# Optimization experiments

Measured on AMD Instinct MI355X. Metric: run time of the kernel, lower is better.

## Reference

```python
import jax, jax.numpy as jnp
import numpy as np

N_NODES = 50000
N_EDGES = 1600000
NODE_DIM = 64
HID = 16


def setup_inputs() -> dict:
    key = jax.random.key(0)
    ks = jax.random.split(key, 12)
    f = lambda k, shape: (jax.random.normal(k, shape, dtype=jnp.float32) * 0.1)
    edge_index = jax.random.randint(ks[0], (2, N_EDGES), 0, N_NODES)
    return {
        "edge_index": edge_index,
        "node_emb": f(ks[1], (N_NODES, NODE_DIM)),
        "edge_emb": f(ks[2], (N_EDGES, HID)),
        "W1": f(ks[3], (NODE_DIM, HID)),
        "att_src1": f(ks[4], (HID,)),
        "att_dst1": f(ks[5], (HID,)),
        "b1": jnp.zeros((HID,), jnp.float32),
        "W2": f(ks[6], (HID, HID)),
        "att_src2": f(ks[7], (HID,)),
        "att_dst2": f(ks[8], (HID,)),
        "b2": jnp.zeros((HID,), jnp.float32),
        "Wm1": f(ks[9], (3 * HID, HID)),
        "bm1": jnp.zeros((HID,), jnp.float32),
        "Wm2": f(ks[10], (HID, 1)),
        "bm2": jnp.zeros((1,), jnp.float32),
    }


def gat_layer(x, src, dst, W, a_src, a_dst, b, num_nodes):
    # Single-head GATConv (PyG defaults): self-loops, leaky_relu(0.2), softmax over dst.
    h = x @ W  # [N, out]
    logits = jax.nn.leaky_relu((h @ a_src)[src] + (h @ a_dst)[dst], negative_slope=0.2)
    m = jax.ops.segment_max(logits, dst, num_segments=num_nodes)  # stable softmax
    e = jnp.exp(logits - jax.lax.stop_gradient(m)[dst])
    denom = jax.ops.segment_sum(e, dst, num_segments=num_nodes)
    coef = e / denom[dst]  # [E+N]
    out = jax.ops.segment_sum(coef[:, None] * h[src], dst, num_segments=num_nodes)
    return out + b


def reference(edge_index, node_emb, edge_emb, W1, att_src1, att_dst1, b1,
              W2, att_src2, att_dst2, b2, Wm1, bm1, Wm2, bm2):
    src, dst = edge_index[0], edge_index[1]
    num_nodes = node_emb.shape[0]
    loops = jnp.arange(num_nodes)
    src_f = jnp.concatenate([src, loops])  # GATConv add_self_loops=True
    dst_f = jnp.concatenate([dst, loops])

    x = node_emb
    for (W, a_s, a_d, b) in [(W1, att_src1, att_dst1, b1), (W2, att_src2, att_dst2, b2)]:
        x = gat_layer(x, src_f, dst_f, W, a_s, a_d, b, num_nodes)
        x = jax.nn.gelu(x, approximate=False)  # torch F.gelu default = exact erf
        # dropout omitted (eval mode)

    # Vectorized replacement of the per-edge Python loop:
    edge_repr = jnp.concatenate([x[src], x[dst], edge_emb], axis=1)  # [E, 3*HID]
    hmid = jax.nn.relu(edge_repr @ Wm1 + bm1)
    probs = jax.nn.sigmoid(hmid @ Wm2 + bm2)[:, 0]  # [E]
    return probs
```

## Files before the change

kernel.cpp:

```cpp
#include <hip/hip_runtime.h>
#include <math.h>

#define N_NODES 50000
#define N_EDGES 1600000
#define NODE_DIM 64
#define HID 16
#define BSZ 64
#define NBUCK ((N_NODES + BSZ - 1) / BSZ)
#define CAPB 2560
#define EPB 2048
#define APB 256
#define APPEND_BLOCKS ((N_EDGES + EPB - 1) / EPB)

typedef _Float16 h8 __attribute__((ext_vector_type(8)));

__global__ void append_kernel(const int* __restrict__ ei,
                              int* __restrict__ gcount,
                              unsigned int* __restrict__ blist) {
    __shared__ int lcount[NBUCK];
    __shared__ int gbase[NBUCK];
    __shared__ int loff[NBUCK];
    int t = threadIdx.x;
    for (int b = t; b < NBUCK; b += APB) { lcount[b] = 0; loff[b] = 0; }
    __syncthreads();
    long base = (long)blockIdx.x * EPB;
#pragma unroll
    for (int k = 0; k < EPB / APB; k++) {
        long i = base + k * APB + t;
        if (i < N_EDGES) atomicAdd(&lcount[ei[N_EDGES + i] >> 6], 1);
    }
    __syncthreads();
    for (int b = t; b < NBUCK; b += APB) {
        int c = lcount[b];
        gbase[b] = c ? atomicAdd(&gcount[b], c) : 0;
    }
    __syncthreads();
#pragma unroll
    for (int k = 0; k < EPB / APB; k++) {
        long i = base + k * APB + t;
        if (i < N_EDGES) {
            int s = ei[i], d = ei[N_EDGES + i];
            int b = d >> 6;
            int pos = gbase[b] + atomicAdd(&loff[b], 1);
            if (pos < CAPB)
                blist[(size_t)b * CAPB + pos] = ((unsigned)(d & 63) << 16) | (unsigned)s;
        }
    }
}

__global__ void sort_kernel(const int* __restrict__ gcount, const unsigned int* __restrict__ blist,
                            unsigned short* __restrict__ csr, int* __restrict__ dstbeg) {
    __shared__ int cnts[BSZ];
    __shared__ int sc[BSZ];
    __shared__ int off[BSZ];
    int b = blockIdx.x, t = threadIdx.x;
    if (t < BSZ) cnts[t] = 0;
    __syncthreads();
    int cnt = gcount[b]; if (cnt > CAPB) cnt = CAPB;
    const unsigned int* lp = blist + (size_t)b * CAPB;
    for (int k = t; k < cnt; k += APB) atomicAdd(&cnts[lp[k] >> 16], 1);
    __syncthreads();
    if (t < BSZ) sc[t] = cnts[t];
    __syncthreads();
    for (int o = 1; o < BSZ; o <<= 1) {
        int v = 0;
        if (t < BSZ && t >= o) v = sc[t - o];
        __syncthreads();
        if (t < BSZ) sc[t] += v;
        __syncthreads();
    }
    if (t < BSZ) {
        int beg = sc[t] - cnts[t];
        off[t] = beg;
        dstbeg[(b << 6) + t] = beg;
    }
    __syncthreads();
    for (int k = t; k < cnt; k += APB) {
        unsigned int r = lp[k];
        int pos = atomicAdd(&off[r >> 16], 1);
        csr[(size_t)b * CAPB + pos] = (unsigned short)(r & 0xFFFF);
    }
}

__global__ void node_h64(const float* __restrict__ x,
                         const float* __restrict__ W,
                         const float* __restrict__ a_src,
                         const float* __restrict__ a_dst,
                         float* __restrict__ h,
                         float* __restrict__ as_, float* __restrict__ ad_) {
    int t = threadIdx.x;
    int n = blockIdx.x * blockDim.x + t;
    if (n >= N_NODES) return;
    float acc[HID];
#pragma unroll
    for (int j = 0; j < HID; j++) acc[j] = 0.f;
    const float4* xr = (const float4*)(x + (size_t)n * NODE_DIM);
#pragma unroll
    for (int k4 = 0; k4 < NODE_DIM / 4; k4++) {
        float4 xv = xr[k4];
        const float* w0 = W + (k4 * 4) * HID;
#pragma unroll
        for (int j = 0; j < HID; j++)
            acc[j] += xv.x * w0[j] + xv.y * w0[HID + j] + xv.z * w0[2 * HID + j] + xv.w * w0[3 * HID + j];
    }
    float s = 0.f, d = 0.f;
#pragma unroll
    for (int j = 0; j < HID; j++) {
        h[(size_t)n * HID + j] = acc[j];
        s += acc[j] * a_src[j];
        d += acc[j] * a_dst[j];
    }
    as_[n] = s; ad_[n] = d;
}

__global__ void gather1_fused(const int* __restrict__ gcount, const int* __restrict__ dstbeg,
                              const unsigned short* __restrict__ csr,
                              const float* __restrict__ h,
                              const float* __restrict__ as_, const float* __restrict__ ad_,
                              const float* __restrict__ b,
                              const float* __restrict__ W2,
                              const float* __restrict__ a_src2,
                              const float* __restrict__ a_dst2,
                              float* __restrict__ h2out,
                              float* __restrict__ as2, float* __restrict__ ad2) {
    int t = threadIdx.x;
    int j = t & 15;
    int half = (t >> 4) & 1;
    float Wcol[HID];
#pragma unroll
    for (int k = 0; k < HID; k++) Wcol[k] = W2[k * HID + j];
    float a2j = a_src2[j], d2j = a_dst2[j], bj = b[j];
    int g = blockIdx.x * (blockDim.x >> 5) + (t >> 5);
    if (g >= N_NODES) return;
    int bk = g >> 6, dl = g & 63;
    int cnt_b = gcount[bk]; if (cnt_b > CAPB) cnt_b = CAPB;
    int beg = dstbeg[g];
    int end = (dl < 63) ? dstbeg[g + 1] : cnt_b;
    if (end > cnt_b) end = cnt_b;
    if (beg > end) beg = end;
    const unsigned short* row = csr + (size_t)bk * CAPB + beg;
    int cnt = end - beg;
    int ch = (cnt + 1) >> 1;
    int lo = half ? ch : 0;
    int hi = half ? cnt : ch;
    float adn = ad_[g];
    float acc = 0.f, den = 0.f;
    int k = lo;
    for (; k + 4 <= hi; k += 4) {
        int s0 = row[k], s1 = row[k + 1], s2 = row[k + 2], s3 = row[k + 3];
        float l0 = as_[s0] + adn, l1 = as_[s1] + adn;
        float l2 = as_[s2] + adn, l3 = as_[s3] + adn;
        l0 = l0 > 0.f ? l0 : 0.2f * l0;
        l1 = l1 > 0.f ? l1 : 0.2f * l1;
        l2 = l2 > 0.f ? l2 : 0.2f * l2;
        l3 = l3 > 0.f ? l3 : 0.2f * l3;
        float e0 = expf(l0), e1 = expf(l1), e2 = expf(l2), e3 = expf(l3);
        float h0 = h[(size_t)s0 * HID + j], h1 = h[(size_t)s1 * HID + j];
        float h2 = h[(size_t)s2 * HID + j], h3 = h[(size_t)s3 * HID + j];
        den += (e0 + e1) + (e2 + e3);
        acc += (e0 * h0 + e1 * h1) + (e2 * h2 + e3 * h3);
    }
    for (; k < hi; k++) {
        int s = row[k];
        float lg = as_[s] + adn;
        lg = lg > 0.f ? lg : 0.2f * lg;
        float e = expf(lg);
        den += e;
        acc += e * h[(size_t)s * HID + j];
    }
    acc += __shfl_xor(acc, 16, 32);
    den += __shfl_xor(den, 16, 32);
    float lg = as_[g] + adn;
    lg = lg > 0.f ? lg : 0.2f * lg;
    float e = expf(lg);
    den += e;
    acc += e * h[(size_t)g * HID + j];
    float v = acc / den + bj;
    v = 0.5f * v * (1.f + erff(v * 0.70710678118654752f));
    float acc2 = 0.f;
#pragma unroll
    for (int k2 = 0; k2 < HID; k2++) {
        float xk = __shfl(v, k2, 16);
        acc2 += xk * Wcol[k2];
    }
    float ps = acc2 * a2j, pd = acc2 * d2j;
#pragma unroll
    for (int o = 1; o < 16; o <<= 1) {
        ps += __shfl_xor(ps, o, 16);
        pd += __shfl_xor(pd, o, 16);
    }
    if (half == 0) {
        h2out[(size_t)g * HID + j] = acc2;
        if (j == 0) { as2[g] = ps; ad2[g] = pd; }
    }
}

__global__ void gather2_fused(const int* __restrict__ gcount, const int* __restrict__ dstbeg,
                              const unsigned short* __restrict__ csr,
                              const float* __restrict__ h,
                              const float* __restrict__ as_, const float* __restrict__ ad_,
                              const float* __restrict__ b,
                              const float* __restrict__ Wm1,
                              const float* __restrict__ bm1,
                              _Float16* __restrict__ A, _Float16* __restrict__ B) {
    int t = threadIdx.x;
    int j = t & 15;
    int half = (t >> 4) & 1;
    float WaC[HID], WbC[HID];
#pragma unroll
    for (int k = 0; k < HID; k++) {
        WaC[k] = Wm1[k * HID + j];
        WbC[k] = Wm1[HID * HID + k * HID + j];
    }
    float bj = b[j], b1j = bm1[j];
    int g = blockIdx.x * (blockDim.x >> 5) + (t >> 5);
    if (g >= N_NODES) return;
    int bk = g >> 6, dl = g & 63;
    int cnt_b = gcount[bk]; if (cnt_b > CAPB) cnt_b = CAPB;
    int beg = dstbeg[g];
    int end = (dl < 63) ? dstbeg[g + 1] : cnt_b;
    if (end > cnt_b) end = cnt_b;
    if (beg > end) beg = end;
    const unsigned short* row = csr + (size_t)bk * CAPB + beg;
    int cnt = end - beg;
    int ch = (cnt + 1) >> 1;
    int lo = half ? ch : 0;
    int hi = half ? cnt : ch;
    float adn = ad_[g];
    float acc = 0.f, den = 0.f;
    int k = lo;
    for (; k + 4 <= hi; k += 4) {
        int s0 = row[k], s1 = row[k + 1], s2 = row[k + 2], s3 = row[k + 3];
        float l0 = as_[s0] + adn, l1 = as_[s1] + adn;
        float l2 = as_[s2] + adn, l3 = as_[s3] + adn;
        l0 = l0 > 0.f ? l0 : 0.2f * l0;
        l1 = l1 > 0.f ? l1 : 0.2f * l1;
        l2 = l2 > 0.f ? l2 : 0.2f * l2;
        l3 = l3 > 0.f ? l3 : 0.2f * l3;
        float e0 = expf(l0), e1 = expf(l1), e2 = expf(l2), e3 = expf(l3);
        float h0 = h[(size_t)s0 * HID + j], h1 = h[(size_t)s1 * HID + j];
        float h2 = h[(size_t)s2 * HID + j], h3 = h[(size_t)s3 * HID + j];
        den += (e0 + e1) + (e2 + e3);
        acc += (e0 * h0 + e1 * h1) + (e2 * h2 + e3 * h3);
    }
    for (; k < hi; k++) {
        int s = row[k];
        float lg = as_[s] + adn;
        lg = lg > 0.f ? lg : 0.2f * lg;
        float e = expf(lg);
        den += e;
        acc += e * h[(size_t)s * HID + j];
    }
    acc += __shfl_xor(acc, 16, 32);
    den += __shfl_xor(den, 16, 32);
    float lg = as_[g] + adn;
    lg = lg > 0.f ? lg : 0.2f * lg;
    float e = expf(lg);
    den += e;
    acc += e * h[(size_t)g * HID + j];
    float v = acc / den + bj;
    v = 0.5f * v * (1.f + erff(v * 0.70710678118654752f));
    float accA = b1j, accB = 0.f;
#pragma unroll
    for (int k2 = 0; k2 < HID; k2++) {
        float xk = __shfl(v, k2, 16);
        accA += xk * WaC[k2];
        accB += xk * WbC[k2];
    }
    if (half == 0) {
        A[(size_t)g * HID + j] = (_Float16)accA;
        B[(size_t)g * HID + j] = (_Float16)accB;
    }
}

__global__ void edge_mlp(const int* __restrict__ ei,
                         const _Float16* __restrict__ A,
                         const _Float16* __restrict__ B,
                         const float* __restrict__ ee,
                         const float* __restrict__ Wm1,
                         const float* __restrict__ Wm2,
                         const float* __restrict__ bm2,
                         float* __restrict__ out) {
    int t = threadIdx.x;
    long i = (long)blockIdx.x * blockDim.x + t;
    if (i >= N_EDGES) return;
    int s = ei[i], d = ei[N_EDGES + i];
    const h8* Ap = (const h8*)(A + (size_t)s * HID);
    const h8* Bp = (const h8*)(B + (size_t)d * HID);
    h8 a0 = Ap[0], a1 = Ap[1];
    h8 b0 = Bp[0], b1 = Bp[1];
    const float4* ep = (const float4*)(ee + (size_t)i * HID);
    float4 e0 = ep[0], e1 = ep[1], e2 = ep[2], e3 = ep[3];
    float a[HID];
#pragma unroll
    for (int j = 0; j < 8; j++) {
        a[j]     = (float)a0[j] + (float)b0[j];
        a[8 + j] = (float)a1[j] + (float)b1[j];
    }
    float ev[HID];
    ev[0]  = e0.x; ev[1]  = e0.y; ev[2]  = e0.z; ev[3]  = e0.w;
    ev[4]  = e1.x; ev[5]  = e1.y; ev[6]  = e1.z; ev[7]  = e1.w;
    ev[8]  = e2.x; ev[9]  = e2.y; ev[10] = e2.z; ev[11] = e2.w;
    ev[12] = e3.x; ev[13] = e3.y; ev[14] = e3.z; ev[15] = e3.w;
    const float4* W4 = (const float4*)(Wm1 + 2 * HID * HID);
#pragma unroll
    for (int k = 0; k < HID; k++) {
        float e1v = ev[k];
        float4 w0 = W4[k * 4 + 0], w1 = W4[k * 4 + 1], w2 = W4[k * 4 + 2], w3 = W4[k * 4 + 3];
        a[0]  += e1v * w0.x; a[1]  += e1v * w0.y; a[2]  += e1v * w0.z; a[3]  += e1v * w0.w;
        a[4]  += e1v * w1.x; a[5]  += e1v * w1.y; a[6]  += e1v * w1.z; a[7]  += e1v * w1.w;
        a[8]  += e1v * w2.x; a[9]  += e1v * w2.y; a[10] += e1v * w2.z; a[11] += e1v * w2.w;
        a[12] += e1v * w3.x; a[13] += e1v * w3.y; a[14] += e1v * w3.z; a[15] += e1v * w3.w;
    }
    float o = bm2[0];
#pragma unroll
    for (int j = 0; j < HID; j++) o += fmaxf(a[j], 0.f) * Wm2[j];
    out[i] = 1.f / (1.f + expf(-o));
}

extern "C" void kernel_launch(void* const* d_in, const int* in_sizes, int n_in,
                              void* d_out, int out_size, void* d_ws, size_t ws_size,
                              hipStream_t stream) {
    const int*   ei       = (const int*)d_in[0];
    const float* node_emb = (const float*)d_in[1];
    const float* edge_emb = (const float*)d_in[2];
    const float* W1       = (const float*)d_in[3];
    const float* att_src1 = (const float*)d_in[4];
    const float* att_dst1 = (const float*)d_in[5];
    const float* b1       = (const float*)d_in[6];
    const float* W2       = (const float*)d_in[7];
    const float* att_src2 = (const float*)d_in[8];
    const float* att_dst2 = (const float*)d_in[9];
    const float* b2       = (const float*)d_in[10];
    const float* Wm1      = (const float*)d_in[11];
    const float* bm1      = (const float*)d_in[12];
    const float* Wm2      = (const float*)d_in[13];
    const float* bm2      = (const float*)d_in[14];
    float* out            = (float*)d_out;

    char* w = (char*)d_ws;
    float*          h      = (float*)w;          w += (size_t)N_NODES * HID * 4;
    float*          h2     = (float*)w;          w += (size_t)N_NODES * HID * 4;
    float*          as_    = (float*)w;          w += (size_t)N_NODES * 4;
    float*          ad_    = (float*)w;          w += (size_t)N_NODES * 4;
    int*            gcount = (int*)w;            w += (size_t)NBUCK * 4;
    unsigned int*   blist  = (unsigned int*)w;   w += (size_t)NBUCK * CAPB * 4;
    unsigned short* csr    = (unsigned short*)w; w += (size_t)NBUCK * CAPB * 2;
    int*            dstbeg = (int*)w;            w += (size_t)NBUCK * BSZ * 4;

    _Float16* Anode = (_Float16*)blist;
    _Float16* Bnode = Anode + (size_t)N_NODES * HID;
    float*    as2   = (float*)(Bnode + (size_t)N_NODES * HID);
    float*    ad2   = as2 + N_NODES;

    const int BT = 256;
    int nblk_node = (N_NODES + BT - 1) / BT;
    int nblk_E    = (N_EDGES + BT - 1) / BT;
    int nblk_g32  = (N_NODES + (BT >> 5) - 1) / (BT >> 5);

    hipMemsetAsync(gcount, 0, (size_t)NBUCK * sizeof(int), stream);
    append_kernel<<<APPEND_BLOCKS, APB, 0, stream>>>(ei, gcount, blist);
    sort_kernel<<<NBUCK, APB, 0, stream>>>(gcount, blist, csr, dstbeg);

    node_h64<<<nblk_node, BT, 0, stream>>>(node_emb, W1, att_src1, att_dst1, h, as_, ad_);
    gather1_fused<<<nblk_g32, BT, 0, stream>>>(gcount, dstbeg, csr, h, as_, ad_, b1,
                                               W2, att_src2, att_dst2, h2, as2, ad2);

    gather2_fused<<<nblk_g32, BT, 0, stream>>>(gcount, dstbeg, csr, h2, as2, ad2, b2,
                                               Wm1, bm1, Anode, Bnode);

    edge_mlp<<<nblk_E, BT, 0, stream>>>(ei, Anode, Bnode, edge_emb, Wm1, Wm2, bm2, out);
}
```

Measured before the change: 355.1 us.

## Replace bucketed CSR build with count/scan/place and cooperative lane gather

Replaces the two-pass bucket append plus per-bucket sort with a classic CSR build: global atomic counting per destination node, a single-block prefix scan, then atomic placement of source indices. It also rewrites the gather loop so each of the 16 lanes computes one edge's attention weight and broadcasts index and weight via shuffles, instead of every lane redundantly computing exp for every edge. The single-block scan and global per-node atomics on a contended array may add serialization, while removing the bucket capacity cap.

```diff
diff --git a/kernel.cpp b/kernel.cpp
--- a/kernel.cpp
+++ b/kernel.cpp
@@ -5,81 +5,52 @@
 #define N_EDGES 1600000
 #define NODE_DIM 64
 #define HID 16
-#define BSZ 64
-#define NBUCK ((N_NODES + BSZ - 1) / BSZ)
-#define CAPB 2560
-#define EPB 2048
-#define APB 256
-#define APPEND_BLOCKS ((N_EDGES + EPB - 1) / EPB)
 
 typedef _Float16 h8 __attribute__((ext_vector_type(8)));
 
-__global__ void append_kernel(const int* __restrict__ ei,
-                              int* __restrict__ gcount,
-                              unsigned int* __restrict__ blist) {
-    __shared__ int lcount[NBUCK];
-    __shared__ int gbase[NBUCK];
-    __shared__ int loff[NBUCK];
-    int t = threadIdx.x;
-    for (int b = t; b < NBUCK; b += APB) { lcount[b] = 0; loff[b] = 0; }
+__global__ void count_kernel(const int* __restrict__ ei, int* __restrict__ gcount) {
+    long i = (long)blockIdx.x * blockDim.x + threadIdx.x;
+    if (i < N_EDGES) atomicAdd(&gcount[ei[N_EDGES + i]], 1);
+}
+
+__global__ void scan_kernel(int* __restrict__ gcount, int* __restrict__ dstbeg) {
+    __shared__ int part[1024];
+    int t = threadIdx.x;
+    const int C = (N_NODES + 1023) / 1024;
+    int base = t * C;
+    int s = 0;
+    for (int k = 0; k < C; k++) {
+        int i = base + k;
+        if (i < N_NODES) s += gcount[i];
+    }
+    part[t] = s;
     __syncthreads();
-    long base = (long)blockIdx.x * EPB;
-#pragma unroll
-    for (int k = 0; k < EPB / APB; k++) {
-        long i = base + k * APB + t;
-        if (i < N_EDGES) atomicAdd(&lcount[ei[N_EDGES + i] >> 6], 1);
-    }
-    __syncthreads();
-    for (int b = t; b < NBUCK; b += APB) {
-        int c = lcount[b];
-        gbase[b] = c ? atomicAdd(&gcount[b], c) : 0;
-    }
-    __syncthreads();
-#pragma unroll
-    for (int k = 0; k < EPB / APB; k++) {
-        long i = base + k * APB + t;
-        if (i < N_EDGES) {
-            int s = ei[i], d = ei[N_EDGES + i];
-            int b = d >> 6;
-            int pos = gbase[b] + atomicAdd(&loff[b], 1);
-            if (pos < CAPB)
-                blist[(size_t)b * CAPB + pos] = ((unsigned)(d & 63) << 16) | (unsigned)s;
+    for (int o = 1; o < 1024; o <<= 1) {
+        int v = (t >= o) ? part[t - o] : 0;
+        __syncthreads();
+        part[t] += v;
+        __syncthreads();
+    }
+    int run = part[t] - s;
+    for (int k = 0; k < C; k++) {
+        int i = base + k;
+        if (i < N_NODES) {
+            int c = gcount[i];
+            dstbeg[i] = run;
+            gcount[i] = run;
+            run += c;
         }
     }
-}
-
-__global__ void sort_kernel(const int* __restrict__ gcount, const unsigned int* __restrict__ blist,
-                            unsigned short* __restrict__ csr, int* __restrict__ dstbeg) {
-    __shared__ int cnts[BSZ];
-    __shared__ int sc[BSZ];
-    __shared__ int off[BSZ];
-    int b = blockIdx.x, t = threadIdx.x;
-    if (t < BSZ) cnts[t] = 0;
-    __syncthreads();
-    int cnt = gcount[b]; if (cnt > CAPB) cnt = CAPB;
-    const unsigned int* lp = blist + (size_t)b * CAPB;
-    for (int k = t; k < cnt; k += APB) atomicAdd(&cnts[lp[k] >> 16], 1);
-    __syncthreads();
-    if (t < BSZ) sc[t] = cnts[t];
-    __syncthreads();
-    for (int o = 1; o < BSZ; o <<= 1) {
-        int v = 0;
-        if (t < BSZ && t >= o) v = sc[t - o];
-        __syncthreads();
-        if (t < BSZ) sc[t] += v;
-        __syncthreads();
-    }
-    if (t < BSZ) {
-        int beg = sc[t] - cnts[t];
-        off[t] = beg;
-        dstbeg[(b << 6) + t] = beg;
-    }
-    __syncthreads();
-    for (int k = t; k < cnt; k += APB) {
-        unsigned int r = lp[k];
-        int pos = atomicAdd(&off[r >> 16], 1);
-        csr[(size_t)b * CAPB + pos] = (unsigned short)(r & 0xFFFF);
-    }
+    if (t == 1023) dstbeg[N_NODES] = part[1023];
+}
+
+__global__ void place_kernel(const int* __restrict__ ei, int* __restrict__ cursor,
+                             unsigned short* __restrict__ csr) {
+    long i = (long)blockIdx.x * blockDim.x + threadIdx.x;
+    if (i >= N_EDGES) return;
+    int s = ei[i], d = ei[N_EDGES + i];
+    int pos = atomicAdd(&cursor[d], 1);
+    csr[pos] = (unsigned short)s;
 }
 
 __global__ void node_h64(const float* __restrict__ x,
@@ -113,7 +84,39 @@
     as_[n] = s; ad_[n] = d;
 }
 
-__global__ void gather1_fused(const int* __restrict__ gcount, const int* __restrict__ dstbeg,
+__device__ __forceinline__ void gather_core(
+        const unsigned short* __restrict__ row, int lo, int hi, int j,
+        const float* __restrict__ h, const float* __restrict__ as_, float adn,
+        float& acc, float& den) {
+    for (int base = lo; base < hi; base += 16) {
+        int nb = hi - base; if (nb > 16) nb = 16;
+        int idx = base + j;
+        int sj = 0;
+        float ej = 0.f;
+        if (idx < hi) {
+            sj = row[idx];
+            float lg = as_[sj] + adn;
+            lg = lg > 0.f ? lg : 0.2f * lg;
+            ej = expf(lg);
+        }
+        den += ej;
+        int e = 0;
+        for (; e + 2 <= nb; e += 2) {
+            int s0 = __shfl(sj, e, 16),     s1 = __shfl(sj, e + 1, 16);
+            float w0 = __shfl(ej, e, 16),   w1 = __shfl(ej, e + 1, 16);
+            float h0 = h[(size_t)s0 * HID + j];
+            float h1 = h[(size_t)s1 * HID + j];
+            acc += w0 * h0 + w1 * h1;
+        }
+        if (e < nb) {
+            int s0 = __shfl(sj, e, 16);
+            float w0 = __shfl(ej, e, 16);
+            acc += w0 * h[(size_t)s0 * HID + j];
+        }
+    }
+}
+
+__global__ void gather1_fused(const int* __restrict__ dstbeg,
                               const unsigned short* __restrict__ csr,
                               const float* __restrict__ h,
                               const float* __restrict__ as_, const float* __restrict__ ad_,
@@ -132,42 +135,17 @@
     float a2j = a_src2[j], d2j = a_dst2[j], bj = b[j];
     int g = blockIdx.x * (blockDim.x >> 5) + (t >> 5);
     if (g >= N_NODES) return;
-    int bk = g >> 6, dl = g & 63;
-    int cnt_b = gcount[bk]; if (cnt_b > CAPB) cnt_b = CAPB;
-    int beg = dstbeg[g];
-    int end = (dl < 63) ? dstbeg[g + 1] : cnt_b;
-    if (end > cnt_b) end = cnt_b;
-    if (beg > end) beg = end;
-    const unsigned short* row = csr + (size_t)bk * CAPB + beg;
+    int beg = dstbeg[g], end = dstbeg[g + 1];
+    const unsigned short* row = csr + beg;
     int cnt = end - beg;
     int ch = (cnt + 1) >> 1;
     int lo = half ? ch : 0;
     int hi = half ? cnt : ch;
     float adn = ad_[g];
     float acc = 0.f, den = 0.f;
-    int k = lo;
-    for (; k + 4 <= hi; k += 4) {
-        int s0 = row[k], s1 = row[k + 1], s2 = row[k + 2], s3 = row[k + 3];
-        float l0 = as_[s0] + adn, l1 = as_[s1] + adn;
-        float l2 = as_[s2] + adn, l3 = as_[s3] + adn;
-        l0 = l0 > 0.f ? l0 : 0.2f * l0;
-        l1 = l1 > 0.f ? l1 : 0.2f * l1;
-        l2 = l2 > 0.f ? l2 : 0.2f * l2;
-        l3 = l3 > 0.f ? l3 : 0.2f * l3;
-        float e0 = expf(l0), e1 = expf(l1), e2 = expf(l2), e3 = expf(l3);
-        float h0 = h[(size_t)s0 * HID + j], h1 = h[(size_t)s1 * HID + j];
-        float h2 = h[(size_t)s2 * HID + j], h3 = h[(size_t)s3 * HID + j];
-        den += (e0 + e1) + (e2 + e3);
-        acc += (e0 * h0 + e1 * h1) + (e2 * h2 + e3 * h3);
-    }
-    for (; k < hi; k++) {
-        int s = row[k];
-        float lg = as_[s] + adn;
-        lg = lg > 0.f ? lg : 0.2f * lg;
-        float e = expf(lg);
-        den += e;
-        acc += e * h[(size_t)s * HID + j];
-    }
+    gather_core(row, lo, hi, j, h, as_, adn, acc, den);
+#pragma unroll
+    for (int o = 1; o < 16; o <<= 1) den += __shfl_xor(den, o, 16);
     acc += __shfl_xor(acc, 16, 32);
     den += __shfl_xor(den, 16, 32);
     float lg = as_[g] + adn;
@@ -195,7 +173,7 @@
     }
 }
 
-__global__ void gather2_fused(const int* __restrict__ gcount, const int* __restrict__ dstbeg,
+__global__ void gather2_fused(const int* __restrict__ dstbeg,
                               const unsigned short* __restrict__ csr,
                               const float* __restrict__ h,
                               const float* __restrict__ as_, const float* __restrict__ ad_,
@@ -215,42 +193,17 @@
     float bj = b[j], b1j = bm1[j];
     int g = blockIdx.x * (blockDim.x >> 5) + (t >> 5);
     if (g >= N_NODES) return;
-    int bk = g >> 6, dl = g & 63;
-    int cnt_b = gcount[bk]; if (cnt_b > CAPB) cnt_b = CAPB;
-    int beg = dstbeg[g];
-    int end = (dl < 63) ? dstbeg[g + 1] : cnt_b;
-    if (end > cnt_b) end = cnt_b;
-    if (beg > end) beg = end;
-    const unsigned short* row = csr + (size_t)bk * CAPB + beg;
+    int beg = dstbeg[g], end = dstbeg[g + 1];
+    const unsigned short* row = csr + beg;
     int cnt = end - beg;
     int ch = (cnt + 1) >> 1;
     int lo = half ? ch : 0;
     int hi = half ? cnt : ch;
     float adn = ad_[g];
     float acc = 0.f, den = 0.f;
-    int k = lo;
-    for (; k + 4 <= hi; k += 4) {
-        int s0 = row[k], s1 = row[k + 1], s2 = row[k + 2], s3 = row[k + 3];
-        float l0 = as_[s0] + adn, l1 = as_[s1] + adn;
-        float l2 = as_[s2] + adn, l3 = as_[s3] + adn;
-        l0 = l0 > 0.f ? l0 : 0.2f * l0;
-        l1 = l1 > 0.f ? l1 : 0.2f * l1;
-        l2 = l2 > 0.f ? l2 : 0.2f * l2;
-        l3 = l3 > 0.f ? l3 : 0.2f * l3;
-        float e0 = expf(l0), e1 = expf(l1), e2 = expf(l2), e3 = expf(l3);
-        float h0 = h[(size_t)s0 * HID + j], h1 = h[(size_t)s1 * HID + j];
-        float h2 = h[(size_t)s2 * HID + j], h3 = h[(size_t)s3 * HID + j];
-        den += (e0 + e1) + (e2 + e3);
-        acc += (e0 * h0 + e1 * h1) + (e2 * h2 + e3 * h3);
-    }
-    for (; k < hi; k++) {
-        int s = row[k];
-        float lg = as_[s] + adn;
-        lg = lg > 0.f ? lg : 0.2f * lg;
-        float e = expf(lg);
-        den += e;
-        acc += e * h[(size_t)s * HID + j];
-    }
+    gather_core(row, lo, hi, j, h, as_, adn, acc, den);
+#pragma unroll
+    for (int o = 1; o < 16; o <<= 1) den += __shfl_xor(den, o, 16);
     acc += __shfl_xor(acc, 16, 32);
     den += __shfl_xor(den, 16, 32);
     float lg = as_[g] + adn;
@@ -343,30 +296,30 @@
     float*          h2     = (float*)w;          w += (size_t)N_NODES * HID * 4;
     float*          as_    = (float*)w;          w += (size_t)N_NODES * 4;
     float*          ad_    = (float*)w;          w += (size_t)N_NODES * 4;
-    int*            gcount = (int*)w;            w += (size_t)NBUCK * 4;
-    unsigned int*   blist  = (unsigned int*)w;   w += (size_t)NBUCK * CAPB * 4;
-    unsigned short* csr    = (unsigned short*)w; w += (size_t)NBUCK * CAPB * 2;
-    int*            dstbeg = (int*)w;            w += (size_t)NBUCK * BSZ * 4;
-
-    _Float16* Anode = (_Float16*)blist;
-    _Float16* Bnode = Anode + (size_t)N_NODES * HID;
-    float*    as2   = (float*)(Bnode + (size_t)N_NODES * HID);
-    float*    ad2   = as2 + N_NODES;
+    float*          as2    = (float*)w;          w += (size_t)N_NODES * 4;
+    float*          ad2    = (float*)w;          w += (size_t)N_NODES * 4;
+    int*            gcount = (int*)w;            w += (size_t)N_NODES * 4;
+    int*            dstbeg = (int*)w;            w += (size_t)(N_NODES + 1) * 4;
+    unsigned short* csr    = (unsigned short*)w; w += (size_t)N_EDGES * 2;
+    w = (char*)(((size_t)w + 15) & ~(size_t)15);
+    _Float16*       Anode  = (_Float16*)w;       w += (size_t)N_NODES * HID * 2;
+    _Float16*       Bnode  = (_Float16*)w;       w += (size_t)N_NODES * HID * 2;
 
     const int BT = 256;
     int nblk_node = (N_NODES + BT - 1) / BT;
     int nblk_E    = (N_EDGES + BT - 1) / BT;
     int nblk_g32  = (N_NODES + (BT >> 5) - 1) / (BT >> 5);
 
-    hipMemsetAsync(gcount, 0, (size_t)NBUCK * sizeof(int), stream);
-    append_kernel<<<APPEND_BLOCKS, APB, 0, stream>>>(ei, gcount, blist);
-    sort_kernel<<<NBUCK, APB, 0, stream>>>(gcount, blist, csr, dstbeg);
+    hipMemsetAsync(gcount, 0, (size_t)N_NODES * sizeof(int), stream);
+    count_kernel<<<nblk_E, BT, 0, stream>>>(ei, gcount);
+    scan_kernel<<<1, 1024, 0, stream>>>(gcount, dstbeg);
+    place_kernel<<<nblk_E, BT, 0, stream>>>(ei, gcount, csr);
 
     node_h64<<<nblk_node, BT, 0, stream>>>(node_emb, W1, att_src1, att_dst1, h, as_, ad_);
-    gather1_fused<<<nblk_g32, BT, 0, stream>>>(gcount, dstbeg, csr, h, as_, ad_, b1,
+    gather1_fused<<<nblk_g32, BT, 0, stream>>>(dstbeg, csr, h, as_, ad_, b1,
                                                W2, att_src2, att_dst2, h2, as2, ad2);
 
-    gather2_fused<<<nblk_g32, BT, 0, stream>>>(gcount, dstbeg, csr, h2, as2, ad2, b2,
+    gather2_fused<<<nblk_g32, BT, 0, stream>>>(dstbeg, csr, h2, as2, ad2, b2,
                                                Wm1, bm1, Anode, Bnode);
 
     edge_mlp<<<nblk_E, BT, 0, stream>>>(ei, Anode, Bnode, edge_emb, Wm1, Wm2, bm2, out);
```

New measurement: 569.7 us. +60.4%, slower.

## Pack fp16 node features and attention scalars into 64-byte per-node records

Applied to the files above, without the earlier changes.

Node features are now stored as fp16 together with the src/dst attention scalars in one 64-byte record per node. Gathers read a single dword per lane and broadcast values with shuffles, so each neighbour costs one cache line instead of separate loads from the h and as_ arrays. Each destination node now gets one 16-lane group instead of a 32-lane group with split halves, which doubles the number of groups and removes the cross-half reduction. The cost is fp16 precision on intermediate features and extra shuffle work in the inner loop.

```diff
diff --git a/kernel.cpp b/kernel.cpp
--- a/kernel.cpp
+++ b/kernel.cpp
@@ -1,5 +1,6 @@
 #include <hip/hip_runtime.h>
 #include <math.h>
+#include <string.h>
 
 #define N_NODES 50000
 #define N_EDGES 1600000
@@ -11,8 +12,29 @@
 #define EPB 2048
 #define APB 256
 #define APPEND_BLOCKS ((N_EDGES + EPB - 1) / EPB)
+#define RECW 16
 
 typedef _Float16 h8 __attribute__((ext_vector_type(8)));
+
+__device__ __forceinline__ float half_from_word(unsigned int w, int hi) {
+    unsigned short us = hi ? (unsigned short)(w >> 16) : (unsigned short)(w & 0xffffu);
+    _Float16 hv;
+    __builtin_memcpy(&hv, &us, 2);
+    return (float)hv;
+}
+__device__ __forceinline__ unsigned int pack_half2(float a, float b) {
+    _Float16 ha = (_Float16)a, hb = (_Float16)b;
+    unsigned short ua, ub;
+    __builtin_memcpy(&ua, &ha, 2);
+    __builtin_memcpy(&ub, &hb, 2);
+    return (unsigned int)ua | ((unsigned int)ub << 16);
+}
+__device__ __forceinline__ unsigned short half_bits(float a) {
+    _Float16 ha = (_Float16)a;
+    unsigned short ua;
+    __builtin_memcpy(&ua, &ha, 2);
+    return ua;
+}
 
 __global__ void append_kernel(const int* __restrict__ ei,
                               int* __restrict__ gcount,
@@ -86,8 +108,7 @@
                          const float* __restrict__ W,
                          const float* __restrict__ a_src,
                          const float* __restrict__ a_dst,
-                         float* __restrict__ h,
-                         float* __restrict__ as_, float* __restrict__ ad_) {
+                         unsigned int* __restrict__ rec) {
     int t = threadIdx.x;
     int n = blockIdx.x * blockDim.x + t;
     if (n >= N_NODES) return;
@@ -106,31 +127,79 @@
     float s = 0.f, d = 0.f;
 #pragma unroll
     for (int j = 0; j < HID; j++) {
-        h[(size_t)n * HID + j] = acc[j];
         s += acc[j] * a_src[j];
         d += acc[j] * a_dst[j];
     }
-    as_[n] = s; ad_[n] = d;
+    uint4 d0, d1;
+    d0.x = pack_half2(acc[0], acc[1]);  d0.y = pack_half2(acc[2], acc[3]);
+    d0.z = pack_half2(acc[4], acc[5]);  d0.w = pack_half2(acc[6], acc[7]);
+    d1.x = pack_half2(acc[8], acc[9]);  d1.y = pack_half2(acc[10], acc[11]);
+    d1.z = pack_half2(acc[12], acc[13]); d1.w = pack_half2(acc[14], acc[15]);
+    uint4* rp = (uint4*)(rec + (size_t)n * RECW);
+    rp[0] = d0;
+    rp[1] = d1;
+    rec[(size_t)n * RECW + 8] = __float_as_uint(s);
+    rec[(size_t)n * RECW + 9] = __float_as_uint(d);
+}
+
+__device__ __forceinline__ void gather_rec(
+        const unsigned short* __restrict__ row, int cnt, int j, int idx, int hi_sel,
+        const unsigned int* __restrict__ rec, float adn,
+        float& acc, float& den) {
+    int k = 0;
+    for (; k + 4 <= cnt; k += 4) {
+        int s0 = row[k], s1 = row[k + 1], s2 = row[k + 2], s3 = row[k + 3];
+        unsigned int w0 = rec[(size_t)s0 * RECW + idx];
+        unsigned int w1 = rec[(size_t)s1 * RECW + idx];
+        unsigned int w2 = rec[(size_t)s2 * RECW + idx];
+        unsigned int w3 = rec[(size_t)s3 * RECW + idx];
+        float a0 = __uint_as_float(__shfl((int)w0, 8, 16));
+        float a1 = __uint_as_float(__shfl((int)w1, 8, 16));
+        float a2 = __uint_as_float(__shfl((int)w2, 8, 16));
+        float a3 = __uint_as_float(__shfl((int)w3, 8, 16));
+        float l0 = a0 + adn, l1 = a1 + adn, l2 = a2 + adn, l3 = a3 + adn;
+        l0 = l0 > 0.f ? l0 : 0.2f * l0;
+        l1 = l1 > 0.f ? l1 : 0.2f * l1;
+        l2 = l2 > 0.f ? l2 : 0.2f * l2;
+        l3 = l3 > 0.f ? l3 : 0.2f * l3;
+        float e0 = expf(l0), e1 = expf(l1), e2 = expf(l2), e3 = expf(l3);
+        float h0 = half_from_word((unsigned int)__shfl((int)w0, j >> 1, 16), hi_sel);
+        float h1 = half_from_word((unsigned int)__shfl((int)w1, j >> 1, 16), hi_sel);
+        float h2 = half_from_word((unsigned int)__shfl((int)w2, j >> 1, 16), hi_sel);
+        float h3 = half_from_word((unsigned int)__shfl((int)w3, j >> 1, 16), hi_sel);
+        den += (e0 + e1) + (e2 + e3);
+        acc += (e0 * h0 + e1 * h1) + (e2 * h2 + e3 * h3);
+    }
+    for (; k < cnt; k++) {
+        int s = row[k];
+        unsigned int w = rec[(size_t)s * RECW + idx];
+        float a = __uint_as_float(__shfl((int)w, 8, 16));
+        float lg = a + adn;
+        lg = lg > 0.f ? lg : 0.2f * lg;
+        float e = expf(lg);
+        float hv = half_from_word((unsigned int)__shfl((int)w, j >> 1, 16), hi_sel);
+        den += e;
+        acc += e * hv;
+    }
 }
 
 __global__ void gather1_fused(const int* __restrict__ gcount, const int* __restrict__ dstbeg,
                               const unsigned short* __restrict__ csr,
-                              const float* __restrict__ h,
-                              const float* __restrict__ as_, const float* __restrict__ ad_,
+                              const unsigned int* __restrict__ rec,
                               const float* __restrict__ b,
                               const float* __restrict__ W2,
                               const float* __restrict__ a_src2,
                               const float* __restrict__ a_dst2,
-                              float* __restrict__ h2out,
-                              float* __restrict__ as2, float* __restrict__ ad2) {
+                              unsigned int* __restrict__ rec2) {
     int t = threadIdx.x;
     int j = t & 15;
-    int half = (t >> 4) & 1;
+    int idx = j < 8 ? j : 8;
+    int hi_sel = j & 1;
     float Wcol[HID];
 #pragma unroll
     for (int k = 0; k < HID; k++) Wcol[k] = W2[k * HID + j];
     float a2j = a_src2[j], d2j = a_dst2[j], bj = b[j];
-    int g = blockIdx.x * (blockDim.x >> 5) + (t >> 5);
+    int g = blockIdx.x * (blockDim.x >> 4) + (t >> 4);
     if (g >= N_NODES) return;
     int bk = g >> 6, dl = g & 63;
     int cnt_b = gcount[bk]; if (cnt_b > CAPB) cnt_b = CAPB;
@@ -140,41 +209,19 @@
     if (beg > end) beg = end;
     const unsigned short* row = csr + (size_t)bk * CAPB + beg;
     int cnt = end - beg;
-    int ch = (cnt + 1) >> 1;
-    int lo = half ? ch : 0;
-    int hi = half ? cnt : ch;
-    float adn = ad_[g];
+    float adn = __uint_as_float(rec[(size_t)g * RECW + 9]);
     float acc = 0.f, den = 0.f;
-    int k = lo;
-    for (; k + 4 <= hi; k += 4) {
-        int s0 = row[k], s1 = row[k + 1], s2 = row[k + 2], s3 = row[k + 3];
-        float l0 = as_[s0] + adn, l1 = as_[s1] + adn;
-        float l2 = as_[s2] + adn, l3 = as_[s3] + adn;
-        l0 = l0 > 0.f ? l0 : 0.2f * l0;
-        l1 = l1 > 0.f ? l1 : 0.2f * l1;
-        l2 = l2 > 0.f ? l2 : 0.2f * l2;
-        l3 = l3 > 0.f ? l3 : 0.2f * l3;
-        float e0 = expf(l0), e1 = expf(l1), e2 = expf(l2), e3 = expf(l3);
-        float h0 = h[(size_t)s0 * HID + j], h1 = h[(size_t)s1 * HID + j];
-        float h2 = h[(size_t)s2 * HID + j], h3 = h[(size_t)s3 * HID + j];
-        den += (e0 + e1) + (e2 + e3);
-        acc += (e0 * h0 + e1 * h1) + (e2 * h2 + e3 * h3);
-    }
-    for (; k < hi; k++) {
-        int s = row[k];
-        float lg = as_[s] + adn;
+    gather_rec(row, cnt, j, idx, hi_sel, rec, adn, acc, den);
+    {
+        unsigned int wg = rec[(size_t)g * RECW + idx];
+        float ag = __uint_as_float(__shfl((int)wg, 8, 16));
+        float lg = ag + adn;
         lg = lg > 0.f ? lg : 0.2f * lg;
         float e = expf(lg);
+        float hg = half_from_word((unsigned int)__shfl((int)wg, j >> 1, 16), hi_sel);
         den += e;
-        acc += e * h[(size_t)s * HID + j];
-    }
-    acc += __shfl_xor(acc, 16, 32);
-    den += __shfl_xor(den, 16, 32);
-    float lg = as_[g] + adn;
-    lg = lg > 0.f ? lg : 0.2f * lg;
-    float e = expf(lg);
-    den += e;
-    acc += e * h[(size_t)g * HID + j];
+        acc += e * hg;
+    }
     float v = acc / den + bj;
     v = 0.5f * v * (1.f + erff(v * 0.70710678118654752f));
     float acc2 = 0.f;
@@ -189,23 +236,24 @@
         ps += __shfl_xor(ps, o, 16);
         pd += __shfl_xor(pd, o, 16);
     }
-    if (half == 0) {
-        h2out[(size_t)g * HID + j] = acc2;
-        if (j == 0) { as2[g] = ps; ad2[g] = pd; }
+    ((unsigned short*)rec2)[(size_t)g * (RECW * 2) + j] = half_bits(acc2);
+    if (j == 0) {
+        rec2[(size_t)g * RECW + 8] = __float_as_uint(ps);
+        rec2[(size_t)g * RECW + 9] = __float_as_uint(pd);
     }
 }
 
 __global__ void gather2_fused(const int* __restrict__ gcount, const int* __restrict__ dstbeg,
                               const unsigned short* __restrict__ csr,
-                              const float* __restrict__ h,
-                              const float* __restrict__ as_, const float* __restrict__ ad_,
+                              const unsigned int* __restrict__ rec2,
                               const float* __restrict__ b,
                               const float* __restrict__ Wm1,
                               const float* __restrict__ bm1,
                               _Float16* __restrict__ A, _Float16* __restrict__ B) {
     int t = threadIdx.x;
     int j = t & 15;
-    int half = (t >> 4) & 1;
+    int idx = j < 8 ? j : 8;
+    int hi_sel = j & 1;
     float WaC[HID], WbC[HID];
 #pragma unroll
     for (int k = 0; k < HID; k++) {
@@ -213,7 +261,7 @@
         WbC[k] = Wm1[HID * HID + k * HID + j];
     }
     float bj = b[j], b1j = bm1[j];
-    int g = blockIdx.x * (blockDim.x >> 5) + (t >> 5);
+    int g = blockIdx.x * (blockDim.x >> 4) + (t >> 4);
     if (g >= N_NODES) return;
     int bk = g >> 6, dl = g & 63;
     int cnt_b = gcount[bk]; if (cnt_b > CAPB) cnt_b = CAPB;
@@ -223,41 +271,19 @@
     if (beg > end) beg = end;
     const unsigned short* row = csr + (size_t)bk * CAPB + beg;
     int cnt = end - beg;
-    int ch = (cnt + 1) >> 1;
-    int lo = half ? ch : 0;
-    int hi = half ? cnt : ch;
-    float adn = ad_[g];
+    float adn = __uint_as_float(rec2[(size_t)g * RECW + 9]);
     float acc = 0.f, den = 0.f;
-    int k = lo;
-    for (; k + 4 <= hi; k += 4) {
-        int s0 = row[k], s1 = row[k + 1], s2 = row[k + 2], s3 = row[k + 3];
-        float l0 = as_[s0] + adn, l1 = as_[s1] + adn;
-        float l2 = as_[s2] + adn, l3 = as_[s3] + adn;
-        l0 = l0 > 0.f ? l0 : 0.2f * l0;
-        l1 = l1 > 0.f ? l1 : 0.2f * l1;
-        l2 = l2 > 0.f ? l2 : 0.2f * l2;
-        l3 = l3 > 0.f ? l3 : 0.2f * l3;
-        float e0 = expf(l0), e1 = expf(l1), e2 = expf(l2), e3 = expf(l3);
-        float h0 = h[(size_t)s0 * HID + j], h1 = h[(size_t)s1 * HID + j];
-        float h2 = h[(size_t)s2 * HID + j], h3 = h[(size_t)s3 * HID + j];
-        den += (e0 + e1) + (e2 + e3);
-        acc += (e0 * h0 + e1 * h1) + (e2 * h2 + e3 * h3);
-    }
-    for (; k < hi; k++) {
-        int s = row[k];
-        float lg = as_[s] + adn;
+    gather_rec(row, cnt, j, idx, hi_sel, rec2, adn, acc, den);
+    {
+        unsigned int wg = rec2[(size_t)g * RECW + idx];
+        float ag = __uint_as_float(__shfl((int)wg, 8, 16));
+        float lg = ag + adn;
         lg = lg > 0.f ? lg : 0.2f * lg;
         float e = expf(lg);
+        float hg = half_from_word((unsigned int)__shfl((int)wg, j >> 1, 16), hi_sel);
         den += e;
-        acc += e * h[(size_t)s * HID + j];
-    }
-    acc += __shfl_xor(acc, 16, 32);
-    den += __shfl_xor(den, 16, 32);
-    float lg = as_[g] + adn;
-    lg = lg > 0.f ? lg : 0.2f * lg;
-    float e = expf(lg);
-    den += e;
-    acc += e * h[(size_t)g * HID + j];
+        acc += e * hg;
+    }
     float v = acc / den + bj;
     v = 0.5f * v * (1.f + erff(v * 0.70710678118654752f));
     float accA = b1j, accB = 0.f;
@@ -267,10 +293,8 @@
         accA += xk * WaC[k2];
         accB += xk * WbC[k2];
     }
-    if (half == 0) {
-        A[(size_t)g * HID + j] = (_Float16)accA;
-        B[(size_t)g * HID + j] = (_Float16)accB;
-    }
+    A[(size_t)g * HID + j] = (_Float16)accA;
+    B[(size_t)g * HID + j] = (_Float16)accB;
 }
 
 __global__ void edge_mlp(const int* __restrict__ ei,
@@ -339,10 +363,8 @@
     float* out            = (float*)d_out;
 
     char* w = (char*)d_ws;
-    float*          h      = (float*)w;          w += (size_t)N_NODES * HID * 4;
-    float*          h2     = (float*)w;          w += (size_t)N_NODES * HID * 4;
-    float*          as_    = (float*)w;          w += (size_t)N_NODES * 4;
-    float*          ad_    = (float*)w;          w += (size_t)N_NODES * 4;
+    unsigned int*   rec1   = (unsigned int*)w;   w += (size_t)N_NODES * RECW * 4;
+    unsigned int*   rec2   = (unsigned int*)w;   w += (size_t)N_NODES * RECW * 4;
     int*            gcount = (int*)w;            w += (size_t)NBUCK * 4;
     unsigned int*   blist  = (unsigned int*)w;   w += (size_t)NBUCK * CAPB * 4;
     unsigned short* csr    = (unsigned short*)w; w += (size_t)NBUCK * CAPB * 2;
@@ -350,24 +372,22 @@
 
     _Float16* Anode = (_Float16*)blist;
     _Float16* Bnode = Anode + (size_t)N_NODES * HID;
-    float*    as2   = (float*)(Bnode + (size_t)N_NODES * HID);
-    float*    ad2   = as2 + N_NODES;
 
     const int BT = 256;
     int nblk_node = (N_NODES + BT - 1) / BT;
     int nblk_E    = (N_EDGES + BT - 1) / BT;
-    int nblk_g32  = (N_NODES + (BT >> 5) - 1) / (BT >> 5);
+    int nblk_g    = (N_NODES * HID + BT - 1) / BT;
 
     hipMemsetAsync(gcount, 0, (size_t)NBUCK * sizeof(int), stream);
     append_kernel<<<APPEND_BLOCKS, APB, 0, stream>>>(ei, gcount, blist);
     sort_kernel<<<NBUCK, APB, 0, stream>>>(gcount, blist, csr, dstbeg);
 
-    node_h64<<<nblk_node, BT, 0, stream>>>(node_emb, W1, att_src1, att_dst1, h, as_, ad_);
-    gather1_fused<<<nblk_g32, BT, 0, stream>>>(gcount, dstbeg, csr, h, as_, ad_, b1,
-                                               W2, att_src2, att_dst2, h2, as2, ad2);
-
-    gather2_fused<<<nblk_g32, BT, 0, stream>>>(gcount, dstbeg, csr, h2, as2, ad2, b2,
-                                               Wm1, bm1, Anode, Bnode);
+    node_h64<<<nblk_node, BT, 0, stream>>>(node_emb, W1, att_src1, att_dst1, rec1);
+    gather1_fused<<<nblk_g, BT, 0, stream>>>(gcount, dstbeg, csr, rec1, b1,
+                                             W2, att_src2, att_dst2, rec2);
+
+    gather2_fused<<<nblk_g, BT, 0, stream>>>(gcount, dstbeg, csr, rec2, b2,
+                                             Wm1, bm1, Anode, Bnode);
 
     edge_mlp<<<nblk_E, BT, 0, stream>>>(ei, Anode, Bnode, edge_emb, Wm1, Wm2, bm2, out);
 }
```

After: 376.4 us. 1.06x slower.
